# Optimization experiments

Hardware: AMD Instinct MI355X
Metric: run time of the kernel (lower is better)

Reference implementation:

```python
import jax, jax.numpy as jnp
import numpy as np

N = 250_000          # total event nodes across the batch
E = 1_000_000        # directed edges (radius-graph style, avg degree 4)
B = 25               # graphs in the batch
BS = N // B          # nodes per graph (contiguous blocks)
NX, NY = 8, 9        # ceil(120/16), ceil(100/12) voxel cells for MaxPooling
NC = NX * NY         # 72 voxel cells per graph
M = B * NC           # pooled node slots (empty cells kept but masked)
GRIDS = 16           # MaxPoolingX: 4x4 cells of size (30,25) over 120x100
NOUT = 2
EPS = 1e-5


def spline_basis(p):
    # SplineConv basis: kernel_size=2 per dim, degree=1 open B-spline, dim=3.
    # basis_s(p) = prod_d (p_d if bit_d(s) else 1 - p_d), s = b0 + 2*b1 + 4*b2
    p = jnp.clip(p, 0.0, 1.0)
    cols = []
    for s in range(8):
        w = jnp.ones(p.shape[0], p.dtype)
        for d in range(3):
            w = w * (p[:, d] if (s >> d) & 1 else 1.0 - p[:, d])
        cols.append(w)
    return jnp.stack(cols, axis=1)  # [E, 8]


def spline_conv(x, src, dst, basis, W, emask, num_nodes):
    # SplineConv with aggr='mean', bias=False, root_weight=False
    xj = x[src]                                   # [E, Cin] gather
    msg = jnp.zeros((xj.shape[0], W.shape[2]), x.dtype)
    for s in range(W.shape[0]):                   # 8 kernel weight matrices
        msg = msg + basis[:, s:s + 1] * (xj @ W[s])
    msg = msg * emask[:, None]
    out = jax.ops.segment_sum(msg, dst, num_segments=num_nodes)
    deg = jax.ops.segment_sum(emask, dst, num_segments=num_nodes)
    return out / jnp.maximum(deg, 1.0)[:, None]


def batch_norm(x, gamma, beta, mask=None):
    # BatchNorm1d over nodes (training-mode batch statistics, biased var)
    if mask is None:
        mean = x.mean(axis=0)
        var = jnp.mean((x - mean) ** 2, axis=0)
        return (x - mean) * jax.lax.rsqrt(var + EPS) * gamma + beta
    m = mask.astype(x.dtype)[:, None]
    cnt = jnp.maximum(m.sum(), 1.0)
    mean = (x * m).sum(axis=0) / cnt
    var = (((x - mean) ** 2) * m).sum(axis=0) / cnt
    return ((x - mean) * jax.lax.rsqrt(var + EPS) * gamma + beta) * m


def _forward(x, pos, edge_attr, ws, gs, bs, fc_w, edge_index, batch):
    src, dst = edge_index[0], edge_index[1]
    basis = spline_basis(edge_attr)
    em = jnp.ones((src.shape[0],), x.dtype)
    for i in range(5):  # conv1..conv5 + norm + relu on the full event graph
        x = spline_conv(x, src, dst, basis, ws[i], em, N)
        x = jax.nn.relu(batch_norm(x, gs[i], bs[i]))
    # ---- MaxPooling: voxel grid (16,12) over pos[:, :2], coarsen graph ----
    cx = jnp.clip(jnp.floor(pos[:, 0] / 16.0).astype(jnp.int32), 0, NX - 1)
    cy = jnp.clip(jnp.floor(pos[:, 1] / 12.0).astype(jnp.int32), 0, NY - 1)
    cluster = batch * NC + cy * NX + cx           # [N] -> [0, M)
    cnt = jax.ops.segment_sum(jnp.ones((N,), x.dtype), cluster, num_segments=M)
    nmask = cnt > 0                               # non-empty voxel cells
    xp = jax.ops.segment_max(x, cluster, num_segments=M)
    xp = jnp.where(nmask[:, None], xp, 0.0)       # [M, 32]
    pp = jax.ops.segment_sum(pos, cluster, num_segments=M) / jnp.maximum(cnt, 1.0)[:, None]
    # coarsen edges: remap via cluster, drop self loops, coalesce duplicates
    key = cluster[src] * M + cluster[dst]
    key = jnp.where(cluster[src] == cluster[dst], M * M, key)
    ks = jnp.sort(key)
    dup = jnp.concatenate([jnp.zeros((1,), bool), ks[1:] == ks[:-1]])
    evalid = (ks < M * M) & (~dup)
    rs = jnp.where(evalid, ks // M, 0)
    cs = jnp.where(evalid, ks % M, 0)
    emf = evalid.astype(x.dtype)
    # Cartesian(norm=True, cat=False) on pooled positions
    d = (pp[cs] - pp[rs]) * emf[:, None]
    maxv = jnp.maximum(jnp.max(jnp.abs(d)), 1e-9)
    ea2 = d / (2.0 * maxv) + 0.5
    basis2 = spline_basis(ea2)
    for i in range(5, 7):  # conv6, conv7 on pooled graph
        xp = spline_conv(xp, rs, cs, basis2, ws[i], emf, M)
        xp = jax.nn.relu(batch_norm(xp, gs[i], bs[i], nmask))
    # ---- MaxPoolingX: (30,25) voxel grid -> 4x4 = 16 cells per graph ----
    bcl = jnp.arange(M, dtype=jnp.int32) // NC    # batch id of each cluster
    gx = jnp.clip(jnp.floor(pp[:, 0] / 30.0).astype(jnp.int32), 0, 3)
    gy = jnp.clip(jnp.floor(pp[:, 1] / 25.0).astype(jnp.int32), 0, 3)
    seg = jnp.where(nmask, bcl * GRIDS + gy * 4 + gx, B * GRIDS)
    xg = jax.ops.segment_max(xp, seg, num_segments=B * GRIDS + 1)[:B * GRIDS]
    xg = jnp.where(jnp.isfinite(xg), xg, 0.0)     # empty cells -> 0
    feat = xg.reshape(B, GRIDS * 32)              # [B, 512]
    return feat @ fc_w.T                          # [B, NOUT]


def setup_inputs() -> dict:
    key = jax.random.key(0)
    k = jax.random.split(key, 16)
    x = jax.random.uniform(k[0], (N, 1), dtype=jnp.float32)
    pos = jax.random.uniform(k[1], (N, 3), dtype=jnp.float32) * jnp.array([120.0, 100.0, 1.0], jnp.float32)
    batch = (jnp.arange(N) // BS).astype(jnp.int32)
    src = jax.random.randint(k[2], (E,), 0, N, dtype=jnp.int32)
    dst = (src // BS) * BS + jax.random.randint(k[3], (E,), 0, BS, dtype=jnp.int32)
    edge_index = jnp.stack([src, dst])
    edge_attr = jax.random.uniform(k[4], (E, 3), dtype=jnp.float32)
    chans = [1, 8, 16, 16, 16, 32, 32, 32]
    inp = {"x": x, "pos": pos, "edge_attr": edge_attr}
    for i in range(7):
        cin, cout = chans[i], chans[i + 1]
        inp[f"w{i+1}"] = jax.random.normal(k[5 + i], (8, cin, cout), jnp.float32) / np.sqrt(8.0 * cin)
    for i in range(7):
        inp[f"g{i+1}"] = jnp.ones((chans[i + 1],), jnp.float32)
    for i in range(7):
        inp[f"b{i+1}"] = jnp.zeros((chans[i + 1],), jnp.float32)
    inp["fc_w"] = jax.random.normal(k[12], (NOUT, GRIDS * 32), jnp.float32) * 0.05
    inp["edge_index"] = edge_index
    inp["batch"] = batch
    return inp


def reference(x, pos, edge_attr, w1, w2, w3, w4, w5, w6, w7,
              g1, g2, g3, g4, g5, g6, g7,
              b1, b2, b3, b4, b5, b6, b7, fc_w, edge_index, batch):
    ws = (w1, w2, w3, w4, w5, w6, w7)
    gs = (g1, g2, g3, g4, g5, g6, g7)
    bs = (b1, b2, b3, b4, b5, b6, b7)
    return _forward(x, pos, edge_attr, ws, gs, bs, fc_w, edge_index, batch)
```

## Files before the change

kernel.cpp:

```cpp
#include <hip/hip_runtime.h>

constexpr int NN   = 250000;
constexpr int NE   = 1000000;
constexpr int NBm  = 25;
constexpr int BSg  = NN / NBm;
constexpr int NCc  = 72;
constexpr int MM   = NBm * NCc;
constexpr int PRES = NBm * NCc * NCc;
constexpr int NBK  = NBm * 16;
constexpr float EPSbn = 1e-5f;


__global__ __launch_bounds__(256) void k_deg(const int* __restrict__ dst, int* __restrict__ deg, int n) {
    int e = blockIdx.x * 256 + threadIdx.x;
    if (e < n) atomicAdd(&deg[dst[e]], 1);
}

__global__ __launch_bounds__(256) void k_dhist(const int* __restrict__ deg, const int* __restrict__ batch,
                                               int* __restrict__ dhist, int n) {
    __shared__ int h[NBK];
    int tid = threadIdx.x;
    for (int i = tid; i < NBK; i += 256) h[i] = 0;
    __syncthreads();
    int i = blockIdx.x * 256 + tid;
    if (i < n) atomicAdd(&h[batch[i] * 16 + min(deg[i], 15)], 1);
    __syncthreads();
    for (int b = tid; b < NBK; b += 256) if (h[b]) atomicAdd(&dhist[b], h[b]);
}

__global__ __launch_bounds__(256) void k_dscan(const int* __restrict__ dhist, int* __restrict__ dcur) {
    __shared__ int tmp[NBK];
    int t = threadIdx.x;
    for (int i = t; i < NBK; i += 256) tmp[i] = dhist[i];
    __syncthreads();
    if (t == 0) { int run = 0; for (int i = 0; i < NBK; i++) { int v = tmp[i]; tmp[i] = run; run += v; } }
    __syncthreads();
    for (int i = t; i < NBK; i += 256) dcur[i] = tmp[i];
}

__global__ __launch_bounds__(256) void k_dscat(const int* __restrict__ deg, const int* __restrict__ batch,
                                               const float* __restrict__ x_in,
                                               int* __restrict__ dcur, int* __restrict__ pinv,
                                               int* __restrict__ deg_p, float* __restrict__ xin_p, int n) {
    __shared__ int lcnt[NBK];
    __shared__ int gbase[NBK];
    int tid = threadIdx.x;
    for (int i = tid; i < NBK; i += 256) lcnt[i] = 0;
    __syncthreads();
    int i = blockIdx.x * 256 + tid;
    int b = 0, rank = 0;
    if (i < n) {
        b = batch[i] * 16 + min(deg[i], 15);
        rank = atomicAdd(&lcnt[b], 1);
    }
    __syncthreads();
    for (int k = tid; k < NBK; k += 256)
        if (lcnt[k]) gbase[k] = atomicAdd(&dcur[k], lcnt[k]);
    __syncthreads();
    if (i < n) {
        int slot = gbase[b] + rank;
        pinv[i] = slot;
        deg_p[slot] = deg[i];
        xin_p[slot] = x_in[i];
    }
}

__global__ __launch_bounds__(256) void k_scan1(const int* __restrict__ in, int n,
                                               int* __restrict__ outEx, int* __restrict__ bsum) {
    __shared__ int lds[256];
    int t = threadIdx.x;
    int base = blockIdx.x * 2048;
    int v[8]; int s = 0;
#pragma unroll
    for (int i = 0; i < 8; i++) { int idx = base + t * 8 + i; v[i] = (idx < n) ? in[idx] : 0; s += v[i]; }
    lds[t] = s; __syncthreads();
    for (int o = 1; o < 256; o <<= 1) {
        int x = (t >= o) ? lds[t - o] : 0; __syncthreads();
        lds[t] += x; __syncthreads();
    }
    if (t == 255) bsum[blockIdx.x] = lds[255];
    int run = lds[t] - s;
#pragma unroll
    for (int i = 0; i < 8; i++) { int idx = base + t * 8 + i; if (idx < n) outEx[idx] = run; run += v[i]; }
}

__global__ __launch_bounds__(256) void k_scan2(int* bsum, int nb) {
    __shared__ int l[256];
    int t = threadIdx.x;
    int v = (t < nb) ? bsum[t] : 0;
    l[t] = v; __syncthreads();
    for (int o = 1; o < 256; o <<= 1) {
        int x = (t >= o) ? l[t - o] : 0; __syncthreads();
        l[t] += x; __syncthreads();
    }
    if (t < nb) bsum[t] = l[t] - v;
}

__global__ __launch_bounds__(256) void k_scan3(int* __restrict__ outEx, int n, const int* __restrict__ bsum) {
    int i = blockIdx.x * 256 + threadIdx.x;
    if (i < n) outEx[i] += bsum[i >> 11];
}

__global__ __launch_bounds__(256) void k_scatter(const int* __restrict__ src, const int* __restrict__ dst,
                                                 const float* __restrict__ ea, const int* __restrict__ offx,
                                                 const int* __restrict__ pinv,
                                                 int* __restrict__ cursor, float4* __restrict__ erec, int n) {
    int e = blockIdx.x * 256 + threadIdx.x;
    if (e >= n) return;
    int d = pinv[dst[e]];
    int j = offx[d] + atomicAdd(&cursor[d], 1);
    float p0 = fminf(fmaxf(ea[e * 3 + 0], 0.f), 1.f);
    float p1 = fminf(fmaxf(ea[e * 3 + 1], 0.f), 1.f);
    float p2 = fminf(fmaxf(ea[e * 3 + 2], 0.f), 1.f);
    erec[j] = make_float4(__int_as_float(pinv[src[e]]), p0, p1, p2);
}

__global__ __launch_bounds__(256) void k_cluster(const float* __restrict__ pos, const int* __restrict__ batch,
                                                 const int* __restrict__ pinv,
                                                 int* __restrict__ cluster, int* __restrict__ cluster_p,
                                                 int* __restrict__ cnt, float* __restrict__ ppsum, int n) {
    int i = blockIdx.x * 256 + threadIdx.x;
    if (i >= n) return;
    float px = pos[i * 3], py = pos[i * 3 + 1], pz = pos[i * 3 + 2];
    int cx = min(max((int)floorf(px / 16.f), 0), 7);
    int cy = min(max((int)floorf(py / 12.f), 0), 8);
    int cl = batch[i] * NCc + cy * 8 + cx;
    cluster[i] = cl;
    cluster_p[pinv[i]] = cl;
    atomicAdd(&cnt[cl], 1);
    atomicAdd(&ppsum[cl * 3 + 0], px);
    atomicAdd(&ppsum[cl * 3 + 1], py);
    atomicAdd(&ppsum[cl * 3 + 2], pz);
}

__global__ __launch_bounds__(256) void k_coarse(const int* __restrict__ src, const int* __restrict__ dst,
                                                const int* __restrict__ cluster, unsigned char* __restrict__ presence,
                                                int n) {
    int e = blockIdx.x * 256 + threadIdx.x;
    if (e >= n) return;
    int r = cluster[src[e]], c = cluster[dst[e]];
    if (r == c) return;
    int g = r / NCc;
    presence[g * (NCc * NCc) + (r % NCc) * NCc + (c % NCc)] = 1;
}

__global__ __launch_bounds__(256) void k_fpp(const int* __restrict__ cnt, const float* __restrict__ ppsum,
                                             float* __restrict__ pp, int* __restrict__ nmask, int* __restrict__ nmc) {
    int m = blockIdx.x * 256 + threadIdx.x;
    if (m >= MM) return;
    int c = cnt[m];
    float inv = 1.f / (float)max(c, 1);
    pp[m * 3 + 0] = ppsum[m * 3 + 0] * inv;
    pp[m * 3 + 1] = ppsum[m * 3 + 1] * inv;
    pp[m * 3 + 2] = ppsum[m * 3 + 2] * inv;
    nmask[m] = (c > 0);
    if (c > 0) atomicAdd(nmc, 1);
}

__global__ __launch_bounds__(256) void k_maxv(const unsigned char* __restrict__ presence, const float* __restrict__ pp,
                                              float* __restrict__ maxv) {
    int i = blockIdx.x * 256 + threadIdx.x;
    float m = 0.f;
    if (i < PRES && presence[i]) {
        int g = i / (NCc * NCc), rem = i % (NCc * NCc);
        int r = g * NCc + rem / NCc, c = g * NCc + rem % NCc;
        float d0 = fabsf(pp[c * 3 + 0] - pp[r * 3 + 0]);
        float d1 = fabsf(pp[c * 3 + 1] - pp[r * 3 + 1]);
        float d2 = fabsf(pp[c * 3 + 2] - pp[r * 3 + 2]);
        m = fmaxf(fmaxf(d0, d1), d2);
    }
    for (int o = 32; o; o >>= 1) m = fmaxf(m, __shfl_xor(m, o));
    if ((threadIdx.x & 63) == 0) atomicMax((int*)maxv, __float_as_int(m));
}


template <int CIN, int COUT, int TPN, bool BN, int BPG>
__global__ __launch_bounds__(256) void k_conv(
    const float* __restrict__ x, const float4* __restrict__ erec,
    const int* __restrict__ off, const int* __restrict__ deg,
    const float* __restrict__ W, const float* __restrict__ st,
    const float* __restrict__ gam, const float* __restrict__ bet, float invcnt,
    float* __restrict__ out, float* __restrict__ stG) {
    constexpr int CPT = CIN / TPN;
    constexpr int SLICE = COUT + 4;
    constexpr int NPB = 512 / TPN;
    constexpr int NH = (COUT > 16) ? 2 : 1;
    constexpr int OH = COUT / NH;
    constexpr int CWH = OH / TPN;
    __shared__ float Ws[8 * CIN * SLICE];
    __shared__ float ssum[COUT], ssq[COUT];
    int tid = threadIdx.x;
    for (int idx = tid; idx < 8 * CIN * COUT; idx += 256) {
        int s = idx / (CIN * COUT), r = idx % (CIN * COUT);
        int ci = r / COUT, co = r % COUT;
        int t_ = ci / CPT, i_ = ci % CPT;
        Ws[((s * CPT + i_) * TPN + t_) * SLICE + co] = W[idx];
    }
    if (tid < COUT) { ssum[tid] = 0.f; ssq[tid] = 0.f; }
    __syncthreads();

    int g = (blockIdx.x & 7) + 8 * ((blockIdx.x >> 3) / BPG);
    int local = (blockIdx.x >> 3) % BPG;
    int t = tid & (TPN - 1);
    int off0 = local * NPB + 2 * (tid / TPN);
    bool act = (g < NBm) && (off0 < BSg);
    int n0 = g * BSg + off0;

    float sc[CPT], sh[CPT];
    if constexpr (BN) {
#pragma unroll
        for (int i = 0; i < CPT; i++) {
            int c = t * CPT + i;
            float mean = st[c] * invcnt;
            float var = st[CIN + c] * invcnt - mean * mean;
            float s = rsqrtf(var + EPSbn) * gam[c];
            sc[i] = s; sh[i] = bet[c] - mean * s;
        }
    }

    float agg[2][8 * CPT];
#pragma unroll
    for (int r = 0; r < 2; r++)
#pragma unroll
        for (int i = 0; i < 8 * CPT; i++) agg[r][i] = 0.f;

    int dgr[2] = {0, 0};
    int jbr[2] = {0, 0};
    if (act) {
        jbr[0] = off[n0];     dgr[0] = deg[n0];
        jbr[1] = off[n0 + 1]; dgr[1] = deg[n0 + 1];
    }
    int mx = max(dgr[0], dgr[1]);
    for (int m = 0; m < mx; m++) {
#pragma unroll
        for (int r = 0; r < 2; r++) {
            if (m < dgr[r]) {
                float4 rec = erec[jbr[r] + m];
                int s = __float_as_int(rec.x);
                float p0 = rec.y, p1 = rec.z, p2 = rec.w;
                float q0 = 1.f - p0, q1 = 1.f - p1, q2 = 1.f - p2;
                float a00 = q0 * q1, a10 = p0 * q1, a01 = q0 * p1, a11 = p0 * p1;
                float bbv[8] = {a00 * q2, a10 * q2, a01 * q2, a11 * q2,
                                a00 * p2, a10 * p2, a01 * p2, a11 * p2};
                const float* xs = &x[(size_t)s * CIN + t * CPT];
                float xv[CPT];
                if constexpr (CPT == 4) {
                    float4 v = *(const float4*)xs;
                    xv[0] = v.x; xv[1] = v.y; xv[2] = v.z; xv[3] = v.w;
                } else {
#pragma unroll
                    for (int i = 0; i < CPT; i++) xv[i] = xs[i];
                }
                if constexpr (BN) {
#pragma unroll
                    for (int i = 0; i < CPT; i++) { float v = xv[i] * sc[i] + sh[i]; xv[i] = v > 0.f ? v : 0.f; }
                }
#pragma unroll
                for (int k = 0; k < 8; k++)
#pragma unroll
                    for (int i = 0; i < CPT; i++) agg[r][k * CPT + i] += bbv[k] * xv[i];
            }
        }
    }

    float inv0 = 1.f / (float)max(dgr[0], 1);
    float inv1 = 1.f / (float)max(dgr[1], 1);

#pragma unroll
    for (int h = 0; h < NH; h++) {
        float o0[OH], o1[OH];
#pragma unroll
        for (int c = 0; c < OH; c++) { o0[c] = 0.f; o1[c] = 0.f; }
#pragma unroll
        for (int k = 0; k < 8; k++)
#pragma unroll
            for (int i = 0; i < CPT; i++) {
                float a0 = agg[0][k * CPT + i];
                float a1 = agg[1][k * CPT + i];
                const float4* wr = (const float4*)&Ws[((k * CPT + i) * TPN + t) * SLICE + h * OH];
#pragma unroll
                for (int c = 0; c < OH / 4; c++) {
                    float4 wv = wr[c];
                    o0[4 * c + 0] += a0 * wv.x; o0[4 * c + 1] += a0 * wv.y;
                    o0[4 * c + 2] += a0 * wv.z; o0[4 * c + 3] += a0 * wv.w;
                    o1[4 * c + 0] += a1 * wv.x; o1[4 * c + 1] += a1 * wv.y;
                    o1[4 * c + 2] += a1 * wv.z; o1[4 * c + 3] += a1 * wv.w;
                }
            }
#pragma unroll
        for (int m = 1; m < TPN; m <<= 1)
#pragma unroll
            for (int c = 0; c < OH; c++) { o0[c] += __shfl_xor(o0[c], m); o1[c] += __shfl_xor(o1[c], m); }

        float v0[CWH], v1[CWH], sv[CWH], qv[CWH];
#pragma unroll
        for (int c = 0; c < CWH; c++) {
            v0[c] = act ? o0[t * CWH + c] * inv0 : 0.f;
            v1[c] = act ? o1[t * CWH + c] * inv1 : 0.f;
            sv[c] = v0[c] + v1[c];
            qv[c] = v0[c] * v0[c] + v1[c] * v1[c];
        }
        if (act) {
            float* op0 = &out[(size_t)n0 * COUT + h * OH + t * CWH];
            float* op1 = op0 + COUT;
#pragma unroll
            for (int c = 0; c < CWH; c++) { op0[c] = v0[c]; op1[c] = v1[c]; }
        }
#pragma unroll
        for (int m = TPN; m < 64; m <<= 1)
#pragma unroll
            for (int c = 0; c < CWH; c++) { sv[c] += __shfl_xor(sv[c], m); qv[c] += __shfl_xor(qv[c], m); }
        if ((tid & 63) < TPN) {
#pragma unroll
            for (int c = 0; c < CWH; c++) {
                atomicAdd(&ssum[h * OH + t * CWH + c], sv[c]);
                atomicAdd(&ssq[h * OH + t * CWH + c], qv[c]);
            }
        }
    }
    __syncthreads();
    if (tid < COUT) atomicAdd(&stG[tid], ssum[tid]);
    else if (tid < 2 * COUT) atomicAdd(&stG[tid], ssq[tid - COUT]);
}

template <int C>
__global__ __launch_bounds__(256) void k_stats(const float* __restrict__ x, int rows, float* __restrict__ st) {
    __shared__ float ls[256], lq[256];
    int t = threadIdx.x;
    int gid = blockIdx.x * 256 + t;
    int c = t % C;
    int r0 = gid / C;
    int rstride = (gridDim.x * 256) / C;
    float s = 0.f, q = 0.f;
    for (int r = r0; r < rows; r += rstride) { float v = x[(size_t)r * C + c]; s += v; q += v * v; }
    ls[t] = s; lq[t] = q;
    __syncthreads();
    if (t < C) {
        float ss = 0.f, qq = 0.f;
        for (int k = t; k < 256; k += C) { ss += ls[k]; qq += lq[k]; }
        atomicAdd(&st[c], ss); atomicAdd(&st[C + c], qq);
    }
}

__global__ __launch_bounds__(256) void k_pool(const float* __restrict__ x, const int* __restrict__ cluster_p,
                                              const float* __restrict__ st, const float* __restrict__ gam,
                                              const float* __restrict__ bet, float invcnt,
                                              float* __restrict__ xp) {
    __shared__ float cellv[NCc * 32];
    __shared__ float scs[32], shs[32];
    int tid = threadIdx.x;
    int g = (blockIdx.x & 7) + 8 * (blockIdx.x >> 6);
    int part = (blockIdx.x >> 3) & 7;
    for (int i = tid; i < NCc * 32; i += 256) cellv[i] = 0.f;
    if (tid < 32) {
        float mean = st[tid] * invcnt;
        float var = st[32 + tid] * invcnt - mean * mean;
        float s = rsqrtf(var + EPSbn) * gam[tid];
        scs[tid] = s; shs[tid] = bet[tid] - mean * s;
    }
    __syncthreads();
    if (g < NBm) {
        int base = g * BSg + part * (BSg / 8);
        const int nelem = (BSg / 8) * 32;
        for (int ii = tid; ii < nelem; ii += 256) {
            int nd = base + (ii >> 5), ch = ii & 31;
            float v = x[(size_t)nd * 32 + ch] * scs[ch] + shs[ch];
            v = v > 0.f ? v : 0.f;
            int lc = cluster_p[nd] - g * NCc;
            atomicMax((int*)&cellv[lc * 32 + ch], __float_as_int(v));
        }
        __syncthreads();
        for (int ii = tid; ii < NCc * 32; ii += 256)
            atomicMax((int*)&xp[g * NCc * 32 + ii], __float_as_int(cellv[ii]));
    }
}

__global__ __launch_bounds__(256) void k_y(const float* __restrict__ xp, const float* __restrict__ W,
                                           float* __restrict__ y) {
    int i = blockIdx.x * 256 + threadIdx.x;
    if (i >= MM * 256) return;
    int r = i >> 8, rem = i & 255, s = rem >> 5, co = rem & 31;
    const float* xr = &xp[r * 32];
    const float* w = &W[s * 1024 + co];
    float a = 0.f;
#pragma unroll
    for (int ci = 0; ci < 32; ci++) a += xr[ci] * w[ci * 32];
    y[i] = a;
}

__global__ __launch_bounds__(256) void k_convp(const float* __restrict__ y, const float* __restrict__ pp,
                                               const unsigned char* __restrict__ presence,
                                               const float* __restrict__ maxv, float* __restrict__ out) {
    int i = blockIdx.x * 256 + threadIdx.x;
    if (i >= MM * 32) return;
    int c = i >> 5, co = i & 31;
    int g = c / NCc, lc = c % NCc;
    float mv = fmaxf(maxv[0], 1e-9f);
    float inv2 = 0.5f / mv;
    float pcx = pp[c * 3], pcy = pp[c * 3 + 1], pcz = pp[c * 3 + 2];
    const unsigned char* pr = &presence[g * (NCc * NCc) + lc];
    float acc = 0.f; int dg = 0;
    for (int lr = 0; lr < NCc; lr++) {
        if (pr[lr * NCc]) {
            dg++;
            int r = g * NCc + lr;
            float p0 = fminf(fmaxf((pcx - pp[r * 3]) * inv2 + 0.5f, 0.f), 1.f);
            float p1 = fminf(fmaxf((pcy - pp[r * 3 + 1]) * inv2 + 0.5f, 0.f), 1.f);
            float p2 = fminf(fmaxf((pcz - pp[r * 3 + 2]) * inv2 + 0.5f, 0.f), 1.f);
            float q0 = 1.f - p0, q1 = 1.f - p1, q2 = 1.f - p2;
            const float* yr = &y[r * 256 + co];
            acc += (q0 * q1 * q2) * yr[0]   + (p0 * q1 * q2) * yr[32]
                 + (q0 * p1 * q2) * yr[64]  + (p0 * p1 * q2) * yr[96]
                 + (q0 * q1 * p2) * yr[128] + (p0 * q1 * p2) * yr[160]
                 + (q0 * p1 * p2) * yr[192] + (p0 * p1 * p2) * yr[224];
        }
    }
    out[i] = acc / (float)max(dg, 1);
}

__global__ __launch_bounds__(256) void k_bnp(float* __restrict__ xp, const float* __restrict__ st,
                                             const float* __restrict__ gam, const float* __restrict__ bet,
                                             const int* __restrict__ nmask, const int* __restrict__ nmc) {
    int i = blockIdx.x * 256 + threadIdx.x;
    if (i >= MM * 32) return;
    int m = i >> 5, ch = i & 31;
    float cnt = (float)max(nmc[0], 1);
    float mean = st[ch] / cnt;
    float var = st[32 + ch] / cnt - mean * mean;
    float s = rsqrtf(var + EPSbn) * gam[ch];
    float v = xp[i] * s + (bet[ch] - mean * s);
    v = v > 0.f ? v : 0.f;
    xp[i] = nmask[m] ? v : 0.f;
}

__global__ __launch_bounds__(256) void k_poolX(const float* __restrict__ xp, const float* __restrict__ pp,
                                               const int* __restrict__ nmask, float* __restrict__ xg) {
    int i = blockIdx.x * 256 + threadIdx.x;
    if (i >= MM * 32) return;
    int m = i >> 5, ch = i & 31;
    if (!nmask[m]) return;
    int g = m / NCc;
    int gx = min(max((int)floorf(pp[m * 3] / 30.f), 0), 3);
    int gy = min(max((int)floorf(pp[m * 3 + 1] / 25.f), 0), 3);
    int seg = g * 16 + gy * 4 + gx;
    atomicMax((int*)&xg[seg * 32 + ch], __float_as_int(xp[i]));
}

__global__ __launch_bounds__(64) void k_fc(const float* __restrict__ xg, const float* __restrict__ fcw,
                                           float* __restrict__ out) {
    int q = blockIdx.x;
    int b = q >> 1, o = q & 1;
    int l = threadIdx.x;
    float a = 0.f;
    for (int k = l; k < 512; k += 64) a += xg[b * 512 + k] * fcw[o * 512 + k];
    for (int s = 32; s; s >>= 1) a += __shfl_xor(a, s);
    if (l == 0) out[b * 2 + o] = a;
}


extern "C" void kernel_launch(void* const* d_in, const int* in_sizes, int n_in,
                              void* d_out, int out_size, void* d_ws, size_t ws_size,
                              hipStream_t stream) {
    const float* x_in  = (const float*)d_in[0];
    const float* pos   = (const float*)d_in[1];
    const float* eattr = (const float*)d_in[2];
    const float* w[7];  for (int i = 0; i < 7; i++) w[i]  = (const float*)d_in[3 + i];
    const float* gm[7]; for (int i = 0; i < 7; i++) gm[i] = (const float*)d_in[10 + i];
    const float* bt[7]; for (int i = 0; i < 7; i++) bt[i] = (const float*)d_in[17 + i];
    const float* fcw   = (const float*)d_in[24];
    const int* ei      = (const int*)d_in[25];
    const int* batch   = (const int*)d_in[26];
    const int* esrc = ei;
    const int* edst = ei + NE;
    float* outp = (float*)d_out;

    char* base = (char*)d_ws;
    size_t cur = 0;
    auto alloc = [&](size_t elems) -> void* {
        void* p = base + cur;
        cur += (((elems * 4) + 255) & ~(size_t)255);
        return p;
    };
    int*   deg_i     = (int*)alloc(NN);
    int*   cursor    = (int*)alloc(NN);
    int*   cnt_i     = (int*)alloc(MM);
    float* ppsum     = (float*)alloc(MM * 3);
    unsigned char* presence = (unsigned char*)alloc(PRES / 4);
    float* maxv      = (float*)alloc(64);
    int*   nmc       = (int*)alloc(64);
    int*   dhist     = (int*)alloc(NBK);
    float* st        = (float*)alloc(7 * 64);
    float* xp_pool   = (float*)alloc(MM * 32);
    float* xg        = (float*)alloc(NBm * 16 * 32);
    size_t zero_bytes = cur;
    int*   off_ex    = (int*)alloc(NN);
    int*   bsum      = (int*)alloc(256);
    int*   cluster   = (int*)alloc(NN);
    int*   cluster_p = (int*)alloc(NN);
    int*   dcur      = (int*)alloc(NBK);
    int*   pinv      = (int*)alloc(NN);
    int*   deg_p     = (int*)alloc(NN);
    float* xin_p     = (float*)alloc(NN);
    float4* erec     = (float4*)alloc((size_t)NE * 4);
    float* x_a       = (float*)alloc((size_t)NN * 32);
    float* x_b       = (float*)alloc((size_t)NN * 16);
    float* pp        = (float*)alloc(MM * 3);
    int*   nmask     = (int*)alloc(MM);
    float* ybuf      = (float*)alloc(MM * 256);
    float* pt0       = (float*)alloc(MM * 32);
    float* pt1       = (float*)alloc(MM * 32);
    (void)ws_size; (void)in_sizes; (void)n_in; (void)out_size;

    (void)hipMemsetAsync(d_ws, 0, zero_bytes, stream);

    int gE = (NE + 255) / 256;
    int gN = (NN + 255) / 256;
    int nbS = (NN + 2047) / 2048;

    k_deg<<<gE, 256, 0, stream>>>(edst, deg_i, NE);
    k_dhist<<<gN, 256, 0, stream>>>(deg_i, batch, dhist, NN);
    k_dscan<<<1, 256, 0, stream>>>(dhist, dcur);
    k_dscat<<<gN, 256, 0, stream>>>(deg_i, batch, x_in, dcur, pinv, deg_p, xin_p, NN);
    k_scan1<<<nbS, 256, 0, stream>>>(deg_p, NN, off_ex, bsum);
    k_scan2<<<1, 256, 0, stream>>>(bsum, nbS);
    k_scan3<<<gN, 256, 0, stream>>>(off_ex, NN, bsum);
    k_scatter<<<gE, 256, 0, stream>>>(esrc, edst, eattr, off_ex, pinv, cursor, erec, NE);
    k_cluster<<<gN, 256, 0, stream>>>(pos, batch, pinv, cluster, cluster_p, cnt_i, ppsum, NN);
    k_coarse<<<gE, 256, 0, stream>>>(esrc, edst, cluster, presence, NE);
    k_fpp<<<(MM + 255) / 256, 256, 0, stream>>>(cnt_i, ppsum, pp, nmask, nmc);
    k_maxv<<<(PRES + 255) / 256, 256, 0, stream>>>(presence, pp, maxv);

    const float invN = 1.f / (float)NN;
    constexpr int BPG1 = (BSg + 511) / 512;
    constexpr int BPG2 = (BSg + 255) / 256;
    constexpr int BPG4 = (BSg + 127) / 128;
    k_conv<1, 8, 1, false, BPG1><<<32 * BPG1, 256, 0, stream>>>(xin_p, erec, off_ex, deg_p,
                                                                w[0], nullptr, nullptr, nullptr, 0.f, x_a, st + 0);
    k_conv<8, 16, 2, true, BPG2><<<32 * BPG2, 256, 0, stream>>>(x_a, erec, off_ex, deg_p,
                                                                w[1], st + 0, gm[0], bt[0], invN, x_b, st + 64);
    k_conv<16, 16, 4, true, BPG4><<<32 * BPG4, 256, 0, stream>>>(x_b, erec, off_ex, deg_p,
                                                                 w[2], st + 64, gm[1], bt[1], invN, x_a, st + 128);
    k_conv<16, 16, 4, true, BPG4><<<32 * BPG4, 256, 0, stream>>>(x_a, erec, off_ex, deg_p,
                                                                 w[3], st + 128, gm[2], bt[2], invN, x_b, st + 192);
    k_conv<16, 32, 4, true, BPG4><<<32 * BPG4, 256, 0, stream>>>(x_b, erec, off_ex, deg_p,
                                                                 w[4], st + 192, gm[3], bt[3], invN, x_a, st + 256);
    k_pool<<<256, 256, 0, stream>>>(x_a, cluster_p, st + 256, gm[4], bt[4], invN, xp_pool);
    k_y<<<(MM * 256 + 255) / 256, 256, 0, stream>>>(xp_pool, w[5], ybuf);
    k_convp<<<(MM * 32 + 255) / 256, 256, 0, stream>>>(ybuf, pp, presence, maxv, pt0);
    k_stats<32><<<8, 256, 0, stream>>>(pt0, MM, st + 320);
    k_bnp<<<(MM * 32 + 255) / 256, 256, 0, stream>>>(pt0, st + 320, gm[5], bt[5], nmask, nmc);
    k_y<<<(MM * 256 + 255) / 256, 256, 0, stream>>>(pt0, w[6], ybuf);
    k_convp<<<(MM * 32 + 255) / 256, 256, 0, stream>>>(ybuf, pp, presence, maxv, pt1);
    k_stats<32><<<8, 256, 0, stream>>>(pt1, MM, st + 384);
    k_bnp<<<(MM * 32 + 255) / 256, 256, 0, stream>>>(pt1, st + 384, gm[6], bt[6], nmask, nmc);
    k_poolX<<<(MM * 32 + 255) / 256, 256, 0, stream>>>(pt1, pp, nmask, xg);
    k_fc<<<50, 64, 0, stream>>>(xg, fcw, outp);
}
```

Baseline: 745.8 us.

## Pair high- and low-degree node chunks per wave to balance conv workload

```diff
diff --git a/kernel.cpp b/kernel.cpp
--- a/kernel.cpp
+++ b/kernel.cpp
@@ -23,7 +23,7 @@
     for (int i = tid; i < NBK; i += 256) h[i] = 0;
     __syncthreads();
     int i = blockIdx.x * 256 + tid;
-    if (i < n) atomicAdd(&h[batch[i] * 16 + min(deg[i], 15)], 1);
+    if (i < n) atomicAdd(&h[batch[i] * 16 + (15 - min(deg[i], 15))], 1);
     __syncthreads();
     for (int b = tid; b < NBK; b += 256) if (h[b]) atomicAdd(&dhist[b], h[b]);
 }
@@ -50,7 +50,7 @@
     int i = blockIdx.x * 256 + tid;
     int b = 0, rank = 0;
     if (i < n) {
-        b = batch[i] * 16 + min(deg[i], 15);
+        b = batch[i] * 16 + (15 - min(deg[i], 15));
         rank = atomicAdd(&lcnt[b], 1);
     }
     __syncthreads();
@@ -174,16 +174,18 @@
 }
 
 
-template <int CIN, int COUT, int TPN, bool BN, int BPG>
+template <int CIN, int COUT, int TPN, bool BN>
 __global__ __launch_bounds__(256) void k_conv(
     const float* __restrict__ x, const float4* __restrict__ erec,
     const int* __restrict__ off, const int* __restrict__ deg,
     const float* __restrict__ W, const float* __restrict__ st,
     const float* __restrict__ gam, const float* __restrict__ bet, float invcnt,
-    float* __restrict__ out, float* __restrict__ stG) {
+    float* __restrict__ out, float* __restrict__ stG, int nwaves) {
     constexpr int CPT = CIN / TPN;
     constexpr int SLICE = COUT + 4;
-    constexpr int NPB = 512 / TPN;
+    constexpr int NPW = 128 / TPN;
+    constexpr int CPG = (BSg + NPW - 1) / NPW;
+    constexpr int WPG = (CPG + 1) / 2;
     constexpr int NH = (COUT > 16) ? 2 : 1;
     constexpr int OH = COUT / NH;
     constexpr int CWH = OH / TPN;
@@ -199,12 +201,13 @@
     if (tid < COUT) { ssum[tid] = 0.f; ssq[tid] = 0.f; }
     __syncthreads();
 
-    int g = (blockIdx.x & 7) + 8 * ((blockIdx.x >> 3) / BPG);
-    int local = (blockIdx.x >> 3) % BPG;
-    int t = tid & (TPN - 1);
-    int off0 = local * NPB + 2 * (tid / TPN);
-    bool act = (g < NBm) && (off0 < BSg);
-    int n0 = g * BSg + off0;
+    int w = blockIdx.x * 4 + (tid >> 6);
+    int lane = tid & 63;
+    int t = lane & (TPN - 1);
+    int qi = lane / TPN;
+    bool wact = (w < nwaves);
+    int g = wact ? (w / WPG) : 0;
+    int p = wact ? (w % WPG) : 0;
 
     float sc[CPT], sh[CPT];
     if constexpr (BN) {
@@ -218,103 +221,114 @@
         }
     }
 
-    float agg[2][8 * CPT];
-#pragma unroll
-    for (int r = 0; r < 2; r++)
-#pragma unroll
-        for (int i = 0; i < 8 * CPT; i++) agg[r][i] = 0.f;
-
-    int dgr[2] = {0, 0};
-    int jbr[2] = {0, 0};
-    if (act) {
-        jbr[0] = off[n0];     dgr[0] = deg[n0];
-        jbr[1] = off[n0 + 1]; dgr[1] = deg[n0 + 1];
-    }
-    int mx = max(dgr[0], dgr[1]);
-    for (int m = 0; m < mx; m++) {
-#pragma unroll
-        for (int r = 0; r < 2; r++) {
-            if (m < dgr[r]) {
-                float4 rec = erec[jbr[r] + m];
-                int s = __float_as_int(rec.x);
-                float p0 = rec.y, p1 = rec.z, p2 = rec.w;
-                float q0 = 1.f - p0, q1 = 1.f - p1, q2 = 1.f - p2;
-                float a00 = q0 * q1, a10 = p0 * q1, a01 = q0 * p1, a11 = p0 * p1;
-                float bbv[8] = {a00 * q2, a10 * q2, a01 * q2, a11 * q2,
-                                a00 * p2, a10 * p2, a01 * p2, a11 * p2};
-                const float* xs = &x[(size_t)s * CIN + t * CPT];
-                float xv[CPT];
-                if constexpr (CPT == 4) {
-                    float4 v = *(const float4*)xs;
-                    xv[0] = v.x; xv[1] = v.y; xv[2] = v.z; xv[3] = v.w;
-                } else {
-#pragma unroll
-                    for (int i = 0; i < CPT; i++) xv[i] = xs[i];
+    for (int rep = 0; rep < 2; rep++) {
+        if (!wact) break;
+        int c = rep ? (CPG - 1 - p) : p;
+        if (rep && c == p) break;
+        int base = g * BSg + c * NPW;
+        int lim = min(NPW, BSg - c * NPW);
+        int no = 2 * qi;
+        bool act = no < lim;
+        int n0 = base + no;
+
+        float agg[2][8 * CPT];
+#pragma unroll
+        for (int r = 0; r < 2; r++)
+#pragma unroll
+            for (int i = 0; i < 8 * CPT; i++) agg[r][i] = 0.f;
+
+        int dgr[2] = {0, 0};
+        int jbr[2] = {0, 0};
+        if (act) {
+            jbr[0] = off[n0];     dgr[0] = deg[n0];
+            jbr[1] = off[n0 + 1]; dgr[1] = deg[n0 + 1];
+        }
+        int mx = max(dgr[0], dgr[1]);
+        for (int m = 0; m < mx; m++) {
+#pragma unroll
+            for (int r = 0; r < 2; r++) {
+                if (m < dgr[r]) {
+                    float4 rec = erec[jbr[r] + m];
+                    int s = __float_as_int(rec.x);
+                    float p0 = rec.y, p1 = rec.z, p2 = rec.w;
+                    float q0 = 1.f - p0, q1 = 1.f - p1, q2 = 1.f - p2;
+                    float a00 = q0 * q1, a10 = p0 * q1, a01 = q0 * p1, a11 = p0 * p1;
+                    float bbv[8] = {a00 * q2, a10 * q2, a01 * q2, a11 * q2,
+                                    a00 * p2, a10 * p2, a01 * p2, a11 * p2};
+                    const float* xs = &x[(size_t)s * CIN + t * CPT];
+                    float xv[CPT];
+                    if constexpr (CPT == 4) {
+                        float4 v = *(const float4*)xs;
+                        xv[0] = v.x; xv[1] = v.y; xv[2] = v.z; xv[3] = v.w;
+                    } else {
+#pragma unroll
+                        for (int i = 0; i < CPT; i++) xv[i] = xs[i];
+                    }
+                    if constexpr (BN) {
+#pragma unroll
+                        for (int i = 0; i < CPT; i++) { float v = xv[i] * sc[i] + sh[i]; xv[i] = v > 0.f ? v : 0.f; }
+                    }
+#pragma unroll
+                    for (int k = 0; k < 8; k++)
+#pragma unroll
+                        for (int i = 0; i < CPT; i++) agg[r][k * CPT + i] += bbv[k] * xv[i];
                 }
-                if constexpr (BN) {
-#pragma unroll
-                    for (int i = 0; i < CPT; i++) { float v = xv[i] * sc[i] + sh[i]; xv[i] = v > 0.f ? v : 0.f; }
-                }
-#pragma unroll
-                for (int k = 0; k < 8; k++)
-#pragma unroll
-                    for (int i = 0; i < CPT; i++) agg[r][k * CPT + i] += bbv[k] * xv[i];
             }
         }
-    }
-
-    float inv0 = 1.f / (float)max(dgr[0], 1);
-    float inv1 = 1.f / (float)max(dgr[1], 1);
-
-#pragma unroll
-    for (int h = 0; h < NH; h++) {
-        float o0[OH], o1[OH];
-#pragma unroll
-        for (int c = 0; c < OH; c++) { o0[c] = 0.f; o1[c] = 0.f; }
-#pragma unroll
-        for (int k = 0; k < 8; k++)
-#pragma unroll
-            for (int i = 0; i < CPT; i++) {
-                float a0 = agg[0][k * CPT + i];
-                float a1 = agg[1][k * CPT + i];
-                const float4* wr = (const float4*)&Ws[((k * CPT + i) * TPN + t) * SLICE + h * OH];
-#pragma unroll
-                for (int c = 0; c < OH / 4; c++) {
-                    float4 wv = wr[c];
-                    o0[4 * c + 0] += a0 * wv.x; o0[4 * c + 1] += a0 * wv.y;
-                    o0[4 * c + 2] += a0 * wv.z; o0[4 * c + 3] += a0 * wv.w;
-                    o1[4 * c + 0] += a1 * wv.x; o1[4 * c + 1] += a1 * wv.y;
-                    o1[4 * c + 2] += a1 * wv.z; o1[4 * c + 3] += a1 * wv.w;
+
+        float inv0 = 1.f / (float)max(dgr[0], 1);
+        float inv1 = 1.f / (float)max(dgr[1], 1);
+
+#pragma unroll
+        for (int h = 0; h < NH; h++) {
+            float o0[OH], o1[OH];
+#pragma unroll
+            for (int c2 = 0; c2 < OH; c2++) { o0[c2] = 0.f; o1[c2] = 0.f; }
+#pragma unroll
+            for (int k = 0; k < 8; k++)
+#pragma unroll
+                for (int i = 0; i < CPT; i++) {
+                    float a0 = agg[0][k * CPT + i];
+                    float a1 = agg[1][k * CPT + i];
+                    const float4* wr = (const float4*)&Ws[((k * CPT + i) * TPN + t) * SLICE + h * OH];
+#pragma unroll
+                    for (int c2 = 0; c2 < OH / 4; c2++) {
+                        float4 wv = wr[c2];
+                        o0[4 * c2 + 0] += a0 * wv.x; o0[4 * c2 + 1] += a0 * wv.y;
+                        o0[4 * c2 + 2] += a0 * wv.z; o0[4 * c2 + 3] += a0 * wv.w;
+                        o1[4 * c2 + 0] += a1 * wv.x; o1[4 * c2 + 1] += a1 * wv.y;
+                        o1[4 * c2 + 2] += a1 * wv.z; o1[4 * c2 + 3] += a1 * wv.w;
+                    }
                 }
+#pragma unroll
+            for (int m = 1; m < TPN; m <<= 1)
+#pragma unroll
+                for (int c2 = 0; c2 < OH; c2++) { o0[c2] += __shfl_xor(o0[c2], m); o1[c2] += __shfl_xor(o1[c2], m); }
+
+            float v0[CWH], v1[CWH], sv[CWH], qv[CWH];
+#pragma unroll
+            for (int c2 = 0; c2 < CWH; c2++) {
+                v0[c2] = act ? o0[t * CWH + c2] * inv0 : 0.f;
+                v1[c2] = act ? o1[t * CWH + c2] * inv1 : 0.f;
+                sv[c2] = v0[c2] + v1[c2];
+                qv[c2] = v0[c2] * v0[c2] + v1[c2] * v1[c2];
             }
-#pragma unroll
-        for (int m = 1; m < TPN; m <<= 1)
-#pragma unroll
-            for (int c = 0; c < OH; c++) { o0[c] += __shfl_xor(o0[c], m); o1[c] += __shfl_xor(o1[c], m); }
-
-        float v0[CWH], v1[CWH], sv[CWH], qv[CWH];
-#pragma unroll
-        for (int c = 0; c < CWH; c++) {
-            v0[c] = act ? o0[t * CWH + c] * inv0 : 0.f;
-            v1[c] = act ? o1[t * CWH + c] * inv1 : 0.f;
-            sv[c] = v0[c] + v1[c];
-            qv[c] = v0[c] * v0[c] + v1[c] * v1[c];
-        }
-        if (act) {
-            float* op0 = &out[(size_t)n0 * COUT + h * OH + t * CWH];
-            float* op1 = op0 + COUT;
-#pragma unroll
-            for (int c = 0; c < CWH; c++) { op0[c] = v0[c]; op1[c] = v1[c]; }
-        }
-#pragma unroll
-        for (int m = TPN; m < 64; m <<= 1)
-#pragma unroll
-            for (int c = 0; c < CWH; c++) { sv[c] += __shfl_xor(sv[c], m); qv[c] += __shfl_xor(qv[c], m); }
-        if ((tid & 63) < TPN) {
-#pragma unroll
-            for (int c = 0; c < CWH; c++) {
-                atomicAdd(&ssum[h * OH + t * CWH + c], sv[c]);
-                atomicAdd(&ssq[h * OH + t * CWH + c], qv[c]);
+            if (act) {
+                float* op0 = &out[(size_t)n0 * COUT + h * OH + t * CWH];
+                float* op1 = op0 + COUT;
+#pragma unroll
+                for (int c2 = 0; c2 < CWH; c2++) { op0[c2] = v0[c2]; op1[c2] = v1[c2]; }
+            }
+#pragma unroll
+            for (int m = TPN; m < 64; m <<= 1)
+#pragma unroll
+                for (int c2 = 0; c2 < CWH; c2++) { sv[c2] += __shfl_xor(sv[c2], m); qv[c2] += __shfl_xor(qv[c2], m); }
+            if (lane < TPN) {
+#pragma unroll
+                for (int c2 = 0; c2 < CWH; c2++) {
+                    atomicAdd(&ssum[h * OH + t * CWH + c2], sv[c2]);
+                    atomicAdd(&ssq[h * OH + t * CWH + c2], qv[c2]);
+                }
             }
         }
     }
@@ -531,19 +545,19 @@
     k_maxv<<<(PRES + 255) / 256, 256, 0, stream>>>(presence, pp, maxv);
 
     const float invN = 1.f / (float)NN;
-    constexpr int BPG1 = (BSg + 511) / 512;
-    constexpr int BPG2 = (BSg + 255) / 256;
-    constexpr int BPG4 = (BSg + 127) / 128;
-    k_conv<1, 8, 1, false, BPG1><<<32 * BPG1, 256, 0, stream>>>(xin_p, erec, off_ex, deg_p,
-                                                                w[0], nullptr, nullptr, nullptr, 0.f, x_a, st + 0);
-    k_conv<8, 16, 2, true, BPG2><<<32 * BPG2, 256, 0, stream>>>(x_a, erec, off_ex, deg_p,
-                                                                w[1], st + 0, gm[0], bt[0], invN, x_b, st + 64);
-    k_conv<16, 16, 4, true, BPG4><<<32 * BPG4, 256, 0, stream>>>(x_b, erec, off_ex, deg_p,
-                                                                 w[2], st + 64, gm[1], bt[1], invN, x_a, st + 128);
-    k_conv<16, 16, 4, true, BPG4><<<32 * BPG4, 256, 0, stream>>>(x_a, erec, off_ex, deg_p,
-                                                                 w[3], st + 128, gm[2], bt[2], invN, x_b, st + 192);
-    k_conv<16, 32, 4, true, BPG4><<<32 * BPG4, 256, 0, stream>>>(x_b, erec, off_ex, deg_p,
-                                                                 w[4], st + 192, gm[3], bt[3], invN, x_a, st + 256);
+    constexpr int W1 = NBm * ((((BSg + 127) / 128) + 1) / 2);
+    constexpr int W2 = NBm * ((((BSg + 63) / 64) + 1) / 2);
+    constexpr int W4 = NBm * ((((BSg + 31) / 32) + 1) / 2);
+    k_conv<1, 8, 1, false><<<(W1 + 3) / 4, 256, 0, stream>>>(xin_p, erec, off_ex, deg_p,
+                                                             w[0], nullptr, nullptr, nullptr, 0.f, x_a, st + 0, W1);
+    k_conv<8, 16, 2, true><<<(W2 + 3) / 4, 256, 0, stream>>>(x_a, erec, off_ex, deg_p,
+                                                             w[1], st + 0, gm[0], bt[0], invN, x_b, st + 64, W2);
+    k_conv<16, 16, 4, true><<<(W4 + 3) / 4, 256, 0, stream>>>(x_b, erec, off_ex, deg_p,
+                                                              w[2], st + 64, gm[1], bt[1], invN, x_a, st + 128, W4);
+    k_conv<16, 16, 4, true><<<(W4 + 3) / 4, 256, 0, stream>>>(x_a, erec, off_ex, deg_p,
+                                                              w[3], st + 128, gm[2], bt[2], invN, x_b, st + 192, W4);
+    k_conv<16, 32, 4, true><<<(W4 + 3) / 4, 256, 0, stream>>>(x_b, erec, off_ex, deg_p,
+                                                              w[4], st + 192, gm[3], bt[3], invN, x_a, st + 256, W4);
     k_pool<<<256, 256, 0, stream>>>(x_a, cluster_p, st + 256, gm[4], bt[4], invN, xp_pool);
     k_y<<<(MM * 256 + 255) / 256, 256, 0, stream>>>(xp_pool, w[5], ybuf);
     k_convp<<<(MM * 32 + 255) / 256, 256, 0, stream>>>(ybuf, pp, presence, maxv, pt0);
```

Result: no change. 747.1 us (+0.2%).
